# Kernel optimization log

Hardware: AMD Instinct MI355X
Metric: run time of the kernel (lower is better)

Reference implementation:

```python
import jax, jax.numpy as jnp
import numpy as np

N_HEADS = 16


def setup_inputs() -> dict:
    key = jax.random.key(0)
    k1, k2, k3 = jax.random.split(key, 3)
    n_embed = 1024
    b, t = 4, 2048
    x = jax.random.normal(k1, (b, t, n_embed), dtype=jnp.float32)
    # Linear weights stored as [in, out]; y = x @ W + b (same math as torch Linear).
    Wqkv = jax.random.normal(k2, (n_embed, 3 * n_embed), dtype=jnp.float32) * (n_embed ** -0.5)
    bqkv = jnp.zeros((3 * n_embed,), dtype=jnp.float32)
    Wout = jax.random.normal(k3, (n_embed, n_embed), dtype=jnp.float32) * (n_embed ** -0.5)
    bout = jnp.zeros((n_embed,), dtype=jnp.float32)
    return {"x": x, "Wqkv": Wqkv, "bqkv": bqkv, "Wout": Wout, "bout": bout}


def reference(x, Wqkv, bqkv, Wout, bout):
    b, t, n_embed = x.shape
    hs = n_embed // N_HEADS
    qkv = x @ Wqkv + bqkv  # [b, t, 3*n_embed]
    q, k, v = jnp.split(qkv, 3, axis=-1)
    # b t (h hs) -> b h t hs
    def to_heads(u):
        return u.reshape(b, t, N_HEADS, hs).transpose(0, 2, 1, 3)
    q, k, v = to_heads(q), to_heads(k), to_heads(v)
    scale = 1.0 / jnp.sqrt(jnp.asarray(hs, dtype=x.dtype))
    scores = jnp.einsum('bhqd,bhkd->bhqk', q, k) * scale  # [b, h, t, t]
    causal = jnp.tril(jnp.ones((t, t), dtype=bool))
    scores = jnp.where(causal, scores, jnp.finfo(scores.dtype).min)
    attn = jax.nn.softmax(scores, axis=-1)
    out = jnp.einsum('bhqk,bhkd->bhqd', attn, v)  # [b, h, t, hs]
    out = out.transpose(0, 2, 1, 3).reshape(b, t, n_embed)  # b h t hs -> b t (h hs)
    return out @ Wout + bout
```

## Files before the change

### kernel.cpp

```cpp
#include <hip/hip_runtime.h>
#include <hip/hip_bf16.h>
#include <stdint.h>

typedef unsigned short u16;
typedef __bf16 bf16x8 __attribute__((ext_vector_type(8)));
typedef float f32x4 __attribute__((ext_vector_type(4)));
typedef u16 ushort8 __attribute__((ext_vector_type(8)));
typedef short short4v __attribute__((ext_vector_type(4)));

__device__ __forceinline__ u16 f2bf(float f) {
    unsigned int u = __builtin_bit_cast(unsigned int, f);
    u += 0x7fffu + ((u >> 16) & 1u);
    return (u16)(u >> 16);
}

#define MFMA16(a, b, c) __builtin_amdgcn_mfma_f32_16x16x32_bf16( \
    __builtin_bit_cast(bf16x8, a), __builtin_bit_cast(bf16x8, b), c, 0, 0, 0)

#if defined(__has_builtin)
#if __has_builtin(__builtin_amdgcn_exp2f)
#define EXP2(x) __builtin_amdgcn_exp2f(x)
#endif
#endif
#ifndef EXP2
#define EXP2(x) __expf((x) * 0.69314718f)
#endif

__device__ __forceinline__ void async16(void* lds, const void* g) {
    __builtin_amdgcn_global_load_lds(
        (const __attribute__((address_space(1))) unsigned int*)(uintptr_t)g,
        (__attribute__((address_space(3))) unsigned int*)(unsigned int)(uintptr_t)lds,
        16, 0, 0);
}

__global__ __launch_bounds__(256) void convert_bf16(
    const float* __restrict__ src, u16* __restrict__ dst)
{
    int i = blockIdx.x * 256 + threadIdx.x;
    float4 f0 = ((const float4*)src)[i * 2];
    float4 f1 = ((const float4*)src)[i * 2 + 1];
    ushort8 v;
    v[0]=f2bf(f0.x); v[1]=f2bf(f0.y); v[2]=f2bf(f0.z); v[3]=f2bf(f0.w);
    v[4]=f2bf(f1.x); v[5]=f2bf(f1.y); v[6]=f2bf(f1.z); v[7]=f2bf(f1.w);
    ((ushort8*)dst)[i] = v;
}

__global__ __launch_bounds__(256) void transpose_convert(
    const float* __restrict__ src, u16* __restrict__ dst, int N, int K)
{
    __shared__ u16 T[64][68];
    const int k0 = blockIdx.x * 64, n0 = blockIdx.y * 64;
    const int tid = threadIdx.x;
    const int rr = tid >> 4, cc = (tid & 15) * 4;
    #pragma unroll
    for (int rnd = 0; rnd < 4; ++rnd) {
        int r = rr + rnd * 16;
        float4 f = *(const float4*)&src[(size_t)(k0 + r) * N + n0 + cc];
        u16 v[4] = {f2bf(f.x), f2bf(f.y), f2bf(f.z), f2bf(f.w)};
        *(unsigned long long*)&T[r][cc] = *(unsigned long long*)v;
    }
    __syncthreads();
    #pragma unroll
    for (int rnd = 0; rnd < 4; ++rnd) {
        int rn = rr + rnd * 16;
        u16 v[4];
        #pragma unroll
        for (int j = 0; j < 4; ++j) v[j] = T[cc + j][rn];
        *(unsigned long long*)&dst[(size_t)(n0 + rn) * K + k0 + cc] =
            *(unsigned long long*)v;
    }
}

__device__ __forceinline__ void gemm_mainloop(
    const u16* __restrict__ A, const u16* __restrict__ Bt,
    u16* As, u16* Bs, int m0, int n0, int tid, f32x4 acc[4][4])
{
    const int lane = tid & 63, w = tid >> 6;
    const int lr = lane & 15, quad = lane >> 4;
    const int wm = w & 1, wn = w >> 1;
    const int grow = lane & 7, gchunk = lane >> 3;

    for (int k0 = 0; k0 < 1024; k0 += 64) {
        __syncthreads();
        #pragma unroll
        for (int r = 0; r < 4; ++r) {
            int rb = w * 4 + r;
            async16(As + rb * 512,
                    A + (size_t)(m0 + rb * 8 + grow) * 1024 + k0 + gchunk * 8);
            async16(Bs + rb * 512,
                    Bt + (size_t)(n0 + rb * 8 + grow) * 1024 + k0 + gchunk * 8);
        }
        __syncthreads();
        #pragma unroll
        for (int kk = 0; kk < 2; ++kk) {
            ushort8 a[4], b[4];
            #pragma unroll
            for (int mt = 0; mt < 4; ++mt) {
                int rb = wm * 8 + mt * 2 + (lr >> 3);
                a[mt] = *(ushort8*)&As[rb * 512 + (kk * 4 + quad) * 64 + (lr & 7) * 8];
            }
            #pragma unroll
            for (int nt = 0; nt < 4; ++nt) {
                int rb = wn * 8 + nt * 2 + (lr >> 3);
                b[nt] = *(ushort8*)&Bs[rb * 512 + (kk * 4 + quad) * 64 + (lr & 7) * 8];
            }
            #pragma unroll
            for (int mt = 0; mt < 4; ++mt)
                #pragma unroll
                for (int nt = 0; nt < 4; ++nt)
                    acc[mt][nt] = MFMA16(a[mt], b[nt], acc[mt][nt]);
        }
    }
}

__global__ __launch_bounds__(256) void qkv_gemm(
    const u16* __restrict__ xb, const u16* __restrict__ Wt,
    const float* __restrict__ bias, u16* __restrict__ qkvb)
{
    __shared__ u16 As[8192], Bs[8192];
    const int m0 = blockIdx.x * 128, n0 = blockIdx.y * 128;
    const int tid = threadIdx.x;
    f32x4 acc[4][4] = {};
    gemm_mainloop(xb, Wt, As, Bs, m0, n0, tid, acc);

    const int lane = tid & 63, w = tid >> 6;
    const int lr = lane & 15, quad = lane >> 4;
    const int wm = w & 1, wn = w >> 1;
    const int which = n0 >> 10;
    float bv[4];
    #pragma unroll
    for (int nt = 0; nt < 4; ++nt) bv[nt] = bias[n0 + wn * 64 + nt * 16 + lr];

    if (which == 2) {
        u16* vT = qkvb + (size_t)2 * 8388608;
        #pragma unroll
        for (int nt = 0; nt < 4; ++nt) {
            int n = n0 + wn * 64 + nt * 16 + lr;
            int hh = (n >> 6) & 15, d = n & 63;
            #pragma unroll
            for (int mt = 0; mt < 4; ++mt) {
                int mbase = m0 + wm * 64 + mt * 16 + quad * 4;
                int b_idx = mbase >> 11, t0 = mbase & 2047;
                short4v o4;
                #pragma unroll
                for (int reg = 0; reg < 4; ++reg)
                    o4[reg] = (short)f2bf(acc[mt][nt][reg] + bv[nt]);
                *(short4v*)&vT[((size_t)(b_idx * 16 + hh) * 64 + d) * 2048 + t0] = o4;
            }
        }
    } else {
        u16* dst = qkvb + (size_t)which * 8388608;
        #pragma unroll
        for (int mt = 0; mt < 4; ++mt)
          #pragma unroll
          for (int nt = 0; nt < 4; ++nt) {
            int n = n0 + wn * 64 + nt * 16 + lr;
            int hh = (n >> 6) & 15, d = n & 63;
            #pragma unroll
            for (int reg = 0; reg < 4; ++reg) {
                int m = m0 + wm * 64 + mt * 16 + quad * 4 + reg;
                int b_idx = m >> 11, t_idx = m & 2047;
                dst[(((size_t)(b_idx * 16 + hh) * 2048 + t_idx) << 6) + d] =
                    f2bf(acc[mt][nt][reg] + bv[nt]);
            }
          }
    }
}

__global__ __launch_bounds__(256) void out_gemm(
    const u16* __restrict__ A, const u16* __restrict__ Wt,
    const float* __restrict__ bias, float* __restrict__ out)
{
    __shared__ u16 As[8192], Bs[8192];
    const int m0 = blockIdx.x * 128, n0 = blockIdx.y * 128;
    const int tid = threadIdx.x;
    f32x4 acc[4][4] = {};
    gemm_mainloop(A, Wt, As, Bs, m0, n0, tid, acc);

    const int lane = tid & 63, w = tid >> 6;
    const int lr = lane & 15, quad = lane >> 4;
    const int wm = w & 1, wn = w >> 1;
    float bv[4];
    #pragma unroll
    for (int nt = 0; nt < 4; ++nt) bv[nt] = bias[n0 + wn * 64 + nt * 16 + lr];
    #pragma unroll
    for (int mt = 0; mt < 4; ++mt)
      #pragma unroll
      for (int nt = 0; nt < 4; ++nt)
        #pragma unroll
        for (int reg = 0; reg < 4; ++reg) {
            int m = m0 + wm * 64 + mt * 16 + quad * 4 + reg;
            int n = n0 + wn * 64 + nt * 16 + lr;
            out[(size_t)m * 1024 + n] = acc[mt][nt][reg] + bv[nt];
        }
}

__global__ __launch_bounds__(256) void attn_kernel(
    const u16* __restrict__ qkvb, u16* __restrict__ o_ws)
{
    const int p = blockIdx.x, h = blockIdx.y, b = blockIdx.z;
    const size_t bh = (size_t)(b * 16 + h) * 131072;
    const u16* Qb = qkvb + bh;
    const u16* Kb = qkvb + 8388608 + bh;
    const u16* Vt = qkvb + 2 * 8388608 + bh;
    __shared__ u16 Ks[2][4096];
    __shared__ u16 Vts[4096];
    __shared__ u16 Ps[64 * 72];
    const int tid = threadIdx.x, lane = tid & 63, w = tid >> 6;
    const int lr = lane & 15, quad = lane >> 4;
    const int grow = lane & 7, gchunk = lane >> 3;
    const float kscale = 0.125f * 1.44269504f;

    for (int pass = 0; pass < 2; ++pass) {
        const int qt = pass ? (31 - p) : p;
        ushort8 qf[2];
        {
            const u16* qr = Qb + (size_t)(qt * 64 + w * 16 + lr) * 64 + quad * 8;
            qf[0] = *(const ushort8*)qr;
            qf[1] = *(const ushort8*)(qr + 32);
        }
        f32x4 o_acc[4] = {};
        float m_i[4], l_i[4];
        #pragma unroll
        for (int r = 0; r < 4; ++r) { m_i[r] = -1e30f; l_i[r] = 0.f; }

        __syncthreads();
        #pragma unroll
        for (int r = 0; r < 2; ++r) {
            int rb = w * 2 + r;
            async16(&Ks[0][rb * 512], Kb + (size_t)(rb * 8 + grow) * 64 + gchunk * 8);
        }

        for (int kt = 0; kt <= qt; ++kt) {
            const int buf = kt & 1;
            __syncthreads();

            #pragma unroll
            for (int r = 0; r < 2; ++r) {
                int rb = w * 2 + r;
                if (kt < qt)
                    async16(&Ks[buf ^ 1][rb * 512],
                            Kb + (size_t)((kt + 1) * 64 + rb * 8 + grow) * 64 + gchunk * 8);
                async16(&Vts[rb * 512],
                        Vt + (size_t)(rb * 8 + grow) * 2048 + kt * 64 + gchunk * 8);
            }

            f32x4 s[4] = {};
            #pragma unroll
            for (int nt = 0; nt < 4; ++nt)
                #pragma unroll
                for (int kk = 0; kk < 2; ++kk) {
                    ushort8 bb = *(ushort8*)&Ks[buf][(nt * 2 + (lr >> 3)) * 512 +
                                                     (kk * 4 + quad) * 64 + (lr & 7) * 8];
                    s[nt] = MFMA16(qf[kk], bb, s[nt]);
                }
            if (kt == qt) {
                #pragma unroll
                for (int nt = 0; nt < 4; ++nt)
                    #pragma unroll
                    for (int reg = 0; reg < 4; ++reg) {
                        int qr = w * 16 + quad * 4 + reg;
                        int kc = nt * 16 + lr;
                        s[nt][reg] = (kc > qr) ? -1e30f : s[nt][reg] * kscale;
                    }
            } else {
                #pragma unroll
                for (int nt = 0; nt < 4; ++nt)
                    #pragma unroll
                    for (int reg = 0; reg < 4; ++reg) s[nt][reg] *= kscale;
            }
            float pr[4][4], alpha[4];
            #pragma unroll
            for (int reg = 0; reg < 4; ++reg) {
                float mx = fmaxf(fmaxf(s[0][reg], s[1][reg]),
                                 fmaxf(s[2][reg], s[3][reg]));
                #pragma unroll
                for (int off = 1; off < 16; off <<= 1)
                    mx = fmaxf(mx, __shfl_xor(mx, off, 64));
                float mnew = fmaxf(m_i[reg], mx);
                alpha[reg] = EXP2(m_i[reg] - mnew);
                m_i[reg] = mnew;
                float rs = 0.f;
                #pragma unroll
                for (int nt = 0; nt < 4; ++nt) {
                    float pv = EXP2(s[nt][reg] - mnew);
                    pr[nt][reg] = pv;
                    rs += pv;
                }
                #pragma unroll
                for (int off = 1; off < 16; off <<= 1)
                    rs += __shfl_xor(rs, off, 64);
                l_i[reg] = l_i[reg] * alpha[reg] + rs;
            }
            #pragma unroll
            for (int dt = 0; dt < 4; ++dt)
                #pragma unroll
                for (int reg = 0; reg < 4; ++reg) o_acc[dt][reg] *= alpha[reg];
            #pragma unroll
            for (int nt = 0; nt < 4; ++nt)
                #pragma unroll
                for (int reg = 0; reg < 4; ++reg)
                    Ps[(w * 16 + quad * 4 + reg) * 72 + nt * 16 + lr] =
                        f2bf(pr[nt][reg]);

            __syncthreads();

            #pragma unroll
            for (int kk = 0; kk < 2; ++kk) {
                ushort8 pa = *(ushort8*)&Ps[(w * 16 + lr) * 72 + kk * 32 + quad * 8];
                #pragma unroll
                for (int dt = 0; dt < 4; ++dt) {
                    ushort8 vb = *(ushort8*)&Vts[(dt * 2 + (lr >> 3)) * 512 +
                                                 (kk * 4 + quad) * 64 + (lr & 7) * 8];
                    o_acc[dt] = MFMA16(pa, vb, o_acc[dt]);
                }
            }
        }

        float rl[4];
        #pragma unroll
        for (int reg = 0; reg < 4; ++reg) rl[reg] = 1.0f / l_i[reg];
        #pragma unroll
        for (int dt = 0; dt < 4; ++dt)
            #pragma unroll
            for (int reg = 0; reg < 4; ++reg) {
                int row = w * 16 + quad * 4 + reg;
                int tq = qt * 64 + row;
                o_ws[((size_t)(b * 2048 + tq) << 10) + h * 64 + dt * 16 + lr] =
                    f2bf(o_acc[dt][reg] * rl[reg]);
            }
    }
}

extern "C" void kernel_launch(void* const* d_in, const int* in_sizes, int n_in,
                              void* d_out, int out_size, void* d_ws, size_t ws_size,
                              hipStream_t stream)
{
    const float* x    = (const float*)d_in[0];
    const float* Wqkv = (const float*)d_in[1];
    const float* bqkv = (const float*)d_in[2];
    const float* Wout = (const float*)d_in[3];
    const float* bout = (const float*)d_in[4];
    float* out = (float*)d_out;

    u16* qkvb = (u16*)d_ws;
    u16* xb   = qkvb + (size_t)3 * 8388608;
    u16* wT   = qkvb + (size_t)4 * 8388608;
    u16* attn_o = xb;

    convert_bf16<<<4096, 256, 0, stream>>>(x, xb);
    transpose_convert<<<dim3(16, 48), 256, 0, stream>>>(Wqkv, wT, 3072, 1024);
    qkv_gemm<<<dim3(64, 24), 256, 0, stream>>>(xb, wT, bqkv, qkvb);
    attn_kernel<<<dim3(16, 16, 4), 256, 0, stream>>>(qkvb, attn_o);
    transpose_convert<<<dim3(16, 16), 256, 0, stream>>>(Wout, wT, 1024, 1024);
    out_gemm<<<dim3(64, 8), 256, 0, stream>>>(attn_o, wT, bout, out);
}
```

Before: 333.4 us.

## Transpose QK^T MFMA layout, lazily rescale softmax, and remap block order

Swaps the MFMA operands so each lane holds a whole query row across its registers. Row max and sum then need only two cross-lane shuffles instead of per-register 16-lane reductions. Adds a lazy rescale: the running max and the output accumulator are updated only when some row's new max exceeds the old one by more than 8 (in log2 units), skipping the exp and multiply work otherwise. Also writes P to shared memory as 64-bit stores and remaps block indices to interleave the work order, at the cost of extra shuffles to broadcast the per-row factors and a wider range for unnormalised values.

```diff
diff --git a/kernel.cpp b/kernel.cpp
--- a/kernel.cpp
+++ b/kernel.cpp
@@ -198,7 +198,9 @@
 __global__ __launch_bounds__(256) void attn_kernel(
     const u16* __restrict__ qkvb, u16* __restrict__ o_ws)
 {
-    const int p = blockIdx.x, h = blockIdx.y, b = blockIdx.z;
+    const int orig = blockIdx.x + 16 * (blockIdx.y + 16 * blockIdx.z);
+    const int work = (orig & 7) * 128 + (orig >> 3);
+    const int p = work & 15, h = (work >> 4) & 15, b = work >> 8;
     const size_t bh = (size_t)(b * 16 + h) * 131072;
     const u16* Qb = qkvb + bh;
     const u16* Kb = qkvb + 8388608 + bh;
@@ -220,9 +222,9 @@
             qf[1] = *(const ushort8*)(qr + 32);
         }
         f32x4 o_acc[4] = {};
-        float m_i[4], l_i[4];
-        #pragma unroll
-        for (int r = 0; r < 4; ++r) { m_i[r] = -1e30f; l_i[r] = 0.f; }
+        float m_i = -1e30f, l_i = 0.f;
+        const int qrow = w * 16 + lr;
+        const int bsrc = (lane & 48) + ((lane >> 4) << 2);
 
         __syncthreads();
         #pragma unroll
@@ -252,16 +254,15 @@
                 for (int kk = 0; kk < 2; ++kk) {
                     ushort8 bb = *(ushort8*)&Ks[buf][(nt * 2 + (lr >> 3)) * 512 +
                                                      (kk * 4 + quad) * 64 + (lr & 7) * 8];
-                    s[nt] = MFMA16(qf[kk], bb, s[nt]);
+                    s[nt] = MFMA16(bb, qf[kk], s[nt]);
                 }
             if (kt == qt) {
                 #pragma unroll
                 for (int nt = 0; nt < 4; ++nt)
                     #pragma unroll
                     for (int reg = 0; reg < 4; ++reg) {
-                        int qr = w * 16 + quad * 4 + reg;
-                        int kc = nt * 16 + lr;
-                        s[nt][reg] = (kc > qr) ? -1e30f : s[nt][reg] * kscale;
+                        int kc = nt * 16 + quad * 4 + reg;
+                        s[nt][reg] = (kc > qrow) ? -1e30f : s[nt][reg] * kscale;
                     }
             } else {
                 #pragma unroll
@@ -269,39 +270,46 @@
                     #pragma unroll
                     for (int reg = 0; reg < 4; ++reg) s[nt][reg] *= kscale;
             }
-            float pr[4][4], alpha[4];
-            #pragma unroll
-            for (int reg = 0; reg < 4; ++reg) {
-                float mx = fmaxf(fmaxf(s[0][reg], s[1][reg]),
-                                 fmaxf(s[2][reg], s[3][reg]));
-                #pragma unroll
-                for (int off = 1; off < 16; off <<= 1)
-                    mx = fmaxf(mx, __shfl_xor(mx, off, 64));
-                float mnew = fmaxf(m_i[reg], mx);
-                alpha[reg] = EXP2(m_i[reg] - mnew);
-                m_i[reg] = mnew;
-                float rs = 0.f;
-                #pragma unroll
-                for (int nt = 0; nt < 4; ++nt) {
-                    float pv = EXP2(s[nt][reg] - mnew);
-                    pr[nt][reg] = pv;
+            float mx = -1e30f;
+            #pragma unroll
+            for (int nt = 0; nt < 4; ++nt)
+                #pragma unroll
+                for (int reg = 0; reg < 4; ++reg) mx = fmaxf(mx, s[nt][reg]);
+            mx = fmaxf(mx, __shfl_xor(mx, 16, 64));
+            mx = fmaxf(mx, __shfl_xor(mx, 32, 64));
+            if (!__all(mx <= m_i + 8.0f)) {
+                float mnew = fmaxf(m_i, mx);
+                float alpha = EXP2(m_i - mnew);
+                m_i = mnew;
+                l_i *= alpha;
+                #pragma unroll
+                for (int reg = 0; reg < 4; ++reg) {
+                    float ar = __shfl(alpha, bsrc + reg, 64);
+                    #pragma unroll
+                    for (int dt = 0; dt < 4; ++dt) o_acc[dt][reg] *= ar;
+                }
+            }
+            float p4[4][4];
+            float rs = 0.f;
+            #pragma unroll
+            for (int nt = 0; nt < 4; ++nt)
+                #pragma unroll
+                for (int reg = 0; reg < 4; ++reg) {
+                    float pv = EXP2(s[nt][reg] - m_i);
+                    p4[nt][reg] = pv;
                     rs += pv;
                 }
-                #pragma unroll
-                for (int off = 1; off < 16; off <<= 1)
-                    rs += __shfl_xor(rs, off, 64);
-                l_i[reg] = l_i[reg] * alpha[reg] + rs;
-            }
-            #pragma unroll
-            for (int dt = 0; dt < 4; ++dt)
-                #pragma unroll
-                for (int reg = 0; reg < 4; ++reg) o_acc[dt][reg] *= alpha[reg];
-            #pragma unroll
-            for (int nt = 0; nt < 4; ++nt)
-                #pragma unroll
-                for (int reg = 0; reg < 4; ++reg)
-                    Ps[(w * 16 + quad * 4 + reg) * 72 + nt * 16 + lr] =
-                        f2bf(pr[nt][reg]);
+            rs += __shfl_xor(rs, 16, 64);
+            rs += __shfl_xor(rs, 32, 64);
+            l_i += rs;
+            #pragma unroll
+            for (int nt = 0; nt < 4; ++nt) {
+                u16 v4[4];
+                #pragma unroll
+                for (int reg = 0; reg < 4; ++reg) v4[reg] = f2bf(p4[nt][reg]);
+                *(unsigned long long*)&Ps[qrow * 72 + nt * 16 + quad * 4] =
+                    *(unsigned long long*)v4;
+            }
 
             __syncthreads();
 
@@ -317,9 +325,10 @@
             }
         }
 
+        float rinv = 1.0f / l_i;
         float rl[4];
         #pragma unroll
-        for (int reg = 0; reg < 4; ++reg) rl[reg] = 1.0f / l_i[reg];
+        for (int reg = 0; reg < 4; ++reg) rl[reg] = __shfl(rinv, bsrc + reg, 64);
         #pragma unroll
         for (int dt = 0; dt < 4; ++dt)
             #pragma unroll
```

Measured after the change: 302.8 us. 1.1x faster.
